# Optimization experiments

Measured on AMD Instinct MI355X. Metric: run time of the kernel, lower is better.

The kernel has to match this reference:

```python
import jax, jax.numpy as jnp
import numpy as np

D = 1024
H = 16
HD = D // H


def setup_inputs() -> dict:
    key = jax.random.key(0)
    ks = jax.random.split(key, 9)
    s = 1.0 / np.sqrt(D)
    x = jax.random.normal(ks[0], (2, 2048, D), dtype=jnp.float32)
    Wq = jax.random.uniform(ks[1], (D, D), jnp.float32, -s, s)
    bq = jax.random.uniform(ks[2], (D,), jnp.float32, -s, s)
    Wk = jax.random.uniform(ks[3], (D, D), jnp.float32, -s, s)
    bk = jax.random.uniform(ks[4], (D,), jnp.float32, -s, s)
    Wv = jax.random.uniform(ks[5], (D, D), jnp.float32, -s, s)
    bv = jax.random.uniform(ks[6], (D,), jnp.float32, -s, s)
    Wo = jax.random.uniform(ks[7], (D, D), jnp.float32, -s, s)
    bo = jax.random.uniform(ks[8], (D,), jnp.float32, -s, s)
    return {"x": x, "Wq": Wq, "bq": bq, "Wk": Wk, "bk": bk,
            "Wv": Wv, "bv": bv, "Wo": Wo, "bo": bo}


def reference(x, Wq, bq, Wk, bk, Wv, bv, Wo, bo):
    B, S, _ = x.shape
    # project and split heads -> [B, H, S, HD]
    def split(t):
        return t.reshape(B, S, H, HD).transpose(0, 2, 1, 3)
    q = split(x @ Wq + bq)
    k = split(x @ Wk + bk)
    v = split(x @ Wv + bv)
    scores = jnp.einsum('bhqd,bhkd->bhqk', q, k) / np.sqrt(HD).astype(np.float32)
    attn = jax.nn.softmax(scores, axis=-1)
    ctx = jnp.einsum('bhqk,bhkd->bhqd', attn, v)  # [B,H,S,HD]
    ctx = ctx.transpose(0, 2, 1, 3).reshape(B, S, D)
    return ctx @ Wo + bo
```

## Files before the change

### kernel.cpp

```cpp
#include <hip/hip_runtime.h>
#include <hip/hip_bf16.h>
#include <math.h>

#define BB 2
#define SS 2048
#define DD 1024
#define HH 16
#define HD 64
#define MM (BB * SS)

typedef __bf16 bf16;
typedef __attribute__((ext_vector_type(8))) __bf16 bf16x8;
typedef __attribute__((ext_vector_type(4))) __bf16 bf16x4;
typedef __attribute__((ext_vector_type(4))) float f32x4;

__device__ __forceinline__ void glds16(const bf16* g, bf16* l) {
    __builtin_amdgcn_global_load_lds(
        (const __attribute__((address_space(1))) void*)g,
        (__attribute__((address_space(3))) void*)l, 16, 0, 0);
}

__global__ __launch_bounds__(256) void cvt_x(const float* __restrict__ x,
                                             bf16* __restrict__ xb) {
    int i = (blockIdx.x * 256 + threadIdx.x) * 4;
    float4 v = *(const float4*)(x + i);
    bf16x4 o;
    o[0] = (bf16)v.x; o[1] = (bf16)v.y; o[2] = (bf16)v.z; o[3] = (bf16)v.w;
    *(bf16x4*)(xb + i) = o;
}

__global__ __launch_bounds__(256) void cvt_w(
    const float* __restrict__ W0, const float* __restrict__ W1,
    const float* __restrict__ W2, const float* __restrict__ W3,
    bf16* __restrict__ Wt) {
    const float* W = (blockIdx.z == 0) ? W0 : (blockIdx.z == 1) ? W1
                   : (blockIdx.z == 2) ? W2 : W3;
    bf16* dst = Wt + (size_t)blockIdx.z * DD * DD;

    __shared__ float T[64][65];
    int k0 = blockIdx.y * 64, n0 = blockIdx.x * 64;
    int tr = threadIdx.x >> 4, tc = (threadIdx.x & 15) * 4;
#pragma unroll
    for (int u = 0; u < 4; u++) {
        int r = tr + u * 16;
        float4 v = *(const float4*)&W[(size_t)(k0 + r) * DD + n0 + tc];
        T[tc + 0][r] = v.x; T[tc + 1][r] = v.y;
        T[tc + 2][r] = v.z; T[tc + 3][r] = v.w;
    }
    __syncthreads();
#pragma unroll
    for (int u = 0; u < 4; u++) {
        int r = tr + u * 16;
        bf16x4 o;
        o[0] = (bf16)T[r][tc + 0]; o[1] = (bf16)T[r][tc + 1];
        o[2] = (bf16)T[r][tc + 2]; o[3] = (bf16)T[r][tc + 3];
        *(bf16x4*)&dst[(size_t)(n0 + r) * DD + k0 + tc] = o;
    }
}

__global__ __launch_bounds__(256) void vt_kernel(const bf16* __restrict__ V,
                                                 bf16* __restrict__ Vt) {
    const int bh = blockIdx.y;
    const int b = bh >> 4, h = bh & 15;
    const int s0 = blockIdx.x * 64;

    __shared__ bf16 T[64][72];
    const int r = threadIdx.x >> 2;
    const int c0 = (threadIdx.x & 3) * 16;

    const bf16* src = V + ((size_t)(b * SS + s0 + r)) * DD + h * HD + c0;
    *(bf16x8*)&T[r][c0]     = *(const bf16x8*)(src);
    *(bf16x8*)&T[r][c0 + 8] = *(const bf16x8*)(src + 8);
    __syncthreads();

    bf16x8 o0, o1;
#pragma unroll
    for (int i = 0; i < 8; i++) o0[i] = T[c0 + i][r];
#pragma unroll
    for (int i = 0; i < 8; i++) o1[i] = T[c0 + 8 + i][r];
    bf16* dst = Vt + ((size_t)bh * HD + r) * SS + s0 + c0;
    *(bf16x8*)dst       = o0;
    *(bf16x8*)(dst + 8) = o1;
}

__global__ __launch_bounds__(256) void mfma_gemm(
    const bf16* __restrict__ A, const bf16* __restrict__ Wt0,
    const float* __restrict__ b0, const float* __restrict__ b1,
    const float* __restrict__ b2,
    bf16* __restrict__ o0, bf16* __restrict__ o1, bf16* __restrict__ o2,
    float* __restrict__ ofp32) {
    const int z = blockIdx.z;
    const bf16* Wt = Wt0 + (size_t)z * DD * DD;
    const float* bias = (z == 0) ? b0 : (z == 1) ? b1 : b2;
    bf16* dstb = (z == 0) ? o0 : (z == 1) ? o1 : o2;

    __shared__ __align__(16) bf16 As[128 * 64];
    __shared__ __align__(16) bf16 Bs[128 * 64];

    const int tid = threadIdx.x;
    const int lane = tid & 63;
    const int w = tid >> 6;
    const int l15 = lane & 15, quad = lane >> 4;
    const int m0 = blockIdx.y * 128;
    const int n0 = blockIdx.x * 128;
    const int mw = (w & 1) * 64;
    const int nw = (w >> 1) * 64;

    f32x4 acc[4][4];
#pragma unroll
    for (int i = 0; i < 4; i++)
#pragma unroll
        for (int j = 0; j < 4; j++) acc[i][j] = (f32x4){0.f, 0.f, 0.f, 0.f};

    for (int kt = 0; kt < DD; kt += 64) {
        __syncthreads();
#pragma unroll
        for (int u = 0; u < 4; u++) {
            int j = tid + u * 256;
            int row = j >> 3, cp = j & 7;
            int c = cp ^ (row & 7);
            glds16(A  + (size_t)(m0 + row) * DD + kt + c * 8, &As[j * 8]);
            glds16(Wt + (size_t)(n0 + row) * DD + kt + c * 8, &Bs[j * 8]);
        }
        __syncthreads();

#pragma unroll
        for (int kh = 0; kh < 2; kh++) {
            bf16x8 af[4], bf[4];
#pragma unroll
            for (int i = 0; i < 4; i++) {
                int ra = mw + i * 16 + l15;
                int ja = ra * 8 + ((kh * 4 + quad) ^ (ra & 7));
                af[i] = *(const bf16x8*)&As[ja * 8];
                int rb = nw + i * 16 + l15;
                int jb = rb * 8 + ((kh * 4 + quad) ^ (rb & 7));
                bf[i] = *(const bf16x8*)&Bs[jb * 8];
            }
#pragma unroll
            for (int i = 0; i < 4; i++)
#pragma unroll
                for (int j = 0; j < 4; j++)
                    acc[i][j] = __builtin_amdgcn_mfma_f32_16x16x32_bf16(
                        af[i], bf[j], acc[i][j], 0, 0, 0);
        }
    }

    float bcol[4];
#pragma unroll
    for (int j = 0; j < 4; j++) bcol[j] = bias[n0 + nw + j * 16 + l15];

    if (ofp32) {
#pragma unroll
        for (int i = 0; i < 4; i++)
#pragma unroll
            for (int j = 0; j < 4; j++)
#pragma unroll
                for (int r = 0; r < 4; r++) {
                    int row = m0 + mw + i * 16 + quad * 4 + r;
                    int col = n0 + nw + j * 16 + l15;
                    ofp32[(size_t)row * DD + col] = acc[i][j][r] + bcol[j];
                }
    } else {
#pragma unroll
        for (int i = 0; i < 4; i++)
#pragma unroll
            for (int j = 0; j < 4; j++)
#pragma unroll
                for (int r = 0; r < 4; r++) {
                    int row = m0 + mw + i * 16 + quad * 4 + r;
                    int col = n0 + nw + j * 16 + l15;
                    dstb[(size_t)row * DD + col] = (bf16)(acc[i][j][r] + bcol[j]);
                }
    }
}

__global__ __launch_bounds__(256) void mfma_attn(
    const bf16* __restrict__ Qb, const bf16* __restrict__ Kb,
    const bf16* __restrict__ Vtg, bf16* __restrict__ ctxb) {
    __shared__ __align__(16) bf16 Qs[64 * 64];
    __shared__ __align__(16) bf16 Ks[64 * 64];
    __shared__ __align__(16) bf16 Vs[64 * 64];
    __shared__ __align__(16) bf16 Ps[4][16 * 64];

    const int tid = threadIdx.x;
    const int lane = tid & 63;
    const int w = tid >> 6;
    const int l15 = lane & 15, quad = lane >> 4;
    const int bh = blockIdx.y;
    const int b = bh >> 4, h = bh & 15;
    const int q0 = blockIdx.x * 64;
    const size_t mb = (size_t)b * SS;
    const int hc = h * HD;
    const bf16* Vt_bh = Vtg + (size_t)bh * HD * SS;
    bf16* Pw = &Ps[w][0];

#pragma unroll
    for (int u = 0; u < 2; u++) {
        int j = tid + u * 256;
        int row = j >> 3, cp = j & 7;
        int c = cp ^ (row & 7);
        glds16(Qb + (mb + q0 + row) * DD + hc + c * 8, &Qs[j * 8]);
    }
    __syncthreads();

    bf16x8 qf[2];
    {
        int rq = w * 16 + l15;
#pragma unroll
        for (int kh = 0; kh < 2; kh++) {
            int jq = rq * 8 + ((kh * 4 + quad) ^ (rq & 7));
            qf[kh] = *(const bf16x8*)&Qs[jq * 8];
        }
    }

    float l_cur = 0.0f;
    f32x4 o[4];
#pragma unroll
    for (int nb = 0; nb < 4; nb++) o[nb] = (f32x4){0.f, 0.f, 0.f, 0.f};

    const float SCL = 0.18033688011112042f;

    int pw_off[4];
#pragma unroll
    for (int kb = 0; kb < 4; kb++) {
        int cw = kb * 2 + (quad >> 1);
        pw_off[kb] = l15 * 64 + ((cw ^ (l15 & 7)) << 3) + (quad & 1) * 4;
    }

    for (int kt = 0; kt < SS; kt += 64) {
        __syncthreads();
#pragma unroll
        for (int u = 0; u < 2; u++) {
            int j = tid + u * 256;
            int row = j >> 3, cp = j & 7;
            int c = cp ^ (row & 7);
            glds16(Kb + (mb + kt + row) * DD + hc + c * 8, &Ks[j * 8]);
            glds16(Vt_bh + (size_t)row * SS + kt + c * 8, &Vs[j * 8]);
        }
        __syncthreads();

        f32x4 sc[4];
#pragma unroll
        for (int kb = 0; kb < 4; kb++) sc[kb] = (f32x4){0.f, 0.f, 0.f, 0.f};
#pragma unroll
        for (int kb = 0; kb < 4; kb++) {
            int rk = kb * 16 + l15;
#pragma unroll
            for (int kh = 0; kh < 2; kh++) {
                int jk = rk * 8 + ((kh * 4 + quad) ^ (rk & 7));
                bf16x8 kf = *(const bf16x8*)&Ks[jk * 8];
                sc[kb] = __builtin_amdgcn_mfma_f32_16x16x32_bf16(
                    kf, qf[kh], sc[kb], 0, 0, 0);
            }
        }

        float rsum = 0.f;
#pragma unroll
        for (int kb = 0; kb < 4; kb++) {
            bf16x4 pvec;
#pragma unroll
            for (int r = 0; r < 4; r++) {
                float p = exp2f(sc[kb][r] * SCL);
                rsum += p;
                pvec[r] = (bf16)p;
            }
            *(bf16x4*)&Pw[pw_off[kb]] = pvec;
        }
        rsum += __shfl_xor(rsum, 16, 64);
        rsum += __shfl_xor(rsum, 32, 64);
        l_cur += rsum;

#pragma unroll
        for (int kh = 0; kh < 2; kh++) {
            bf16x8 pf = *(const bf16x8*)&Pw[l15 * 64 + (((kh * 4 + quad) ^ (l15 & 7)) << 3)];
#pragma unroll
            for (int nb = 0; nb < 4; nb++) {
                int rv = nb * 16 + l15;
                int jv = rv * 8 + ((kh * 4 + quad) ^ (rv & 7));
                bf16x8 vf = *(const bf16x8*)&Vs[jv * 8];
                o[nb] = __builtin_amdgcn_mfma_f32_16x16x32_bf16(
                    pf, vf, o[nb], 0, 0, 0);
            }
        }
    }

    float linv = 1.0f / l_cur;
    float li[4];
#pragma unroll
    for (int r = 0; r < 4; r++) li[r] = __shfl(linv, quad * 4 + r, 64);
#pragma unroll
    for (int nb = 0; nb < 4; nb++)
#pragma unroll
        for (int r = 0; r < 4; r++) {
            int qrow = q0 + w * 16 + quad * 4 + r;
            ctxb[(mb + qrow) * DD + hc + nb * 16 + l15] = (bf16)(o[nb][r] * li[r]);
        }
}

extern "C" void kernel_launch(void* const* d_in, const int* in_sizes, int n_in,
                              void* d_out, int out_size, void* d_ws, size_t ws_size,
                              hipStream_t stream) {
    const float* x  = (const float*)d_in[0];
    const float* Wq = (const float*)d_in[1];
    const float* bq = (const float*)d_in[2];
    const float* Wk = (const float*)d_in[3];
    const float* bk = (const float*)d_in[4];
    const float* Wv = (const float*)d_in[5];
    const float* bv = (const float*)d_in[6];
    const float* Wo = (const float*)d_in[7];
    const float* bo = (const float*)d_in[8];
    float* out = (float*)d_out;

    char* base = (char*)d_ws;
    bf16* xb   = (bf16*)(base);
    bf16* Wt   = (bf16*)(base + (8ull  << 20));
    bf16* Qb   = (bf16*)(base + (16ull << 20));
    bf16* Kb   = (bf16*)(base + (24ull << 20));
    bf16* Vb   = (bf16*)(base + (32ull << 20));
    bf16* ctxb = (bf16*)(base + (40ull << 20));
    bf16* Vtg  = xb;

    cvt_x<<<dim3((MM * DD) / (256 * 4)), dim3(256), 0, stream>>>(x, xb);
    cvt_w<<<dim3(16, 16, 4), dim3(256), 0, stream>>>(Wq, Wk, Wv, Wo, Wt);

    mfma_gemm<<<dim3(DD / 128, MM / 128, 3), dim3(256), 0, stream>>>(
        xb, Wt, bq, bk, bv, Qb, Kb, Vb, nullptr);

    vt_kernel<<<dim3(SS / 64, BB * HH), dim3(256), 0, stream>>>(Vb, Vtg);

    mfma_attn<<<dim3(SS / 64, BB * HH), dim3(256), 0, stream>>>(Qb, Kb, Vtg, ctxb);

    mfma_gemm<<<dim3(DD / 128, MM / 128, 1), dim3(256), 0, stream>>>(
        ctxb, Wt + 3ull * DD * DD, bo, bo, bo, nullptr, nullptr, nullptr, out);
}
```

Measured before the change: 229.8 us.

## Fold softmax scale into Q projection, add 64-row output GEMM, simplify attention addressing

The Q projection epilogue now multiplies by the softmax scale, so the attention inner loop drops one multiply per score. The output projection moves to a dedicated kernel with 64x128 tiles, doubling its grid from 256 to 512 blocks to fill more CUs. In the attention kernel, Q is loaded straight from global memory into registers instead of through shared memory, and the swizzled LDS offsets and global pointers are precomputed outside the KV loop. Scaling Q before the bf16 rounding slightly changes numerics, and the precomputed offsets raise register pressure.

Result: faster. 224.8 us (-2.2%).

```diff
diff --git a/kernel.cpp b/kernel.cpp
--- a/kernel.cpp
+++ b/kernel.cpp
@@ -13,6 +13,8 @@
 typedef __attribute__((ext_vector_type(8))) __bf16 bf16x8;
 typedef __attribute__((ext_vector_type(4))) __bf16 bf16x4;
 typedef __attribute__((ext_vector_type(4))) float f32x4;
+
+#define QSCL 0.18033688011112042f
 
 __device__ __forceinline__ void glds16(const bf16* g, bf16* l) {
     __builtin_amdgcn_global_load_lds(
@@ -87,12 +89,12 @@
     const bf16* __restrict__ A, const bf16* __restrict__ Wt0,
     const float* __restrict__ b0, const float* __restrict__ b1,
     const float* __restrict__ b2,
-    bf16* __restrict__ o0, bf16* __restrict__ o1, bf16* __restrict__ o2,
-    float* __restrict__ ofp32) {
+    bf16* __restrict__ o0, bf16* __restrict__ o1, bf16* __restrict__ o2) {
     const int z = blockIdx.z;
     const bf16* Wt = Wt0 + (size_t)z * DD * DD;
     const float* bias = (z == 0) ? b0 : (z == 1) ? b1 : b2;
     bf16* dstb = (z == 0) ? o0 : (z == 1) ? o1 : o2;
+    const float scl = (z == 0) ? QSCL : 1.0f;
 
     __shared__ __align__(16) bf16 As[128 * 64];
     __shared__ __align__(16) bf16 Bs[128 * 64];
@@ -149,35 +151,99 @@
 #pragma unroll
     for (int j = 0; j < 4; j++) bcol[j] = bias[n0 + nw + j * 16 + l15];
 
-    if (ofp32) {
-#pragma unroll
-        for (int i = 0; i < 4; i++)
-#pragma unroll
-            for (int j = 0; j < 4; j++)
-#pragma unroll
-                for (int r = 0; r < 4; r++) {
-                    int row = m0 + mw + i * 16 + quad * 4 + r;
-                    int col = n0 + nw + j * 16 + l15;
-                    ofp32[(size_t)row * DD + col] = acc[i][j][r] + bcol[j];
-                }
-    } else {
-#pragma unroll
-        for (int i = 0; i < 4; i++)
-#pragma unroll
-            for (int j = 0; j < 4; j++)
-#pragma unroll
-                for (int r = 0; r < 4; r++) {
-                    int row = m0 + mw + i * 16 + quad * 4 + r;
-                    int col = n0 + nw + j * 16 + l15;
-                    dstb[(size_t)row * DD + col] = (bf16)(acc[i][j][r] + bcol[j]);
-                }
-    }
+#pragma unroll
+    for (int i = 0; i < 4; i++)
+#pragma unroll
+        for (int j = 0; j < 4; j++)
+#pragma unroll
+            for (int r = 0; r < 4; r++) {
+                int row = m0 + mw + i * 16 + quad * 4 + r;
+                int col = n0 + nw + j * 16 + l15;
+                dstb[(size_t)row * DD + col] =
+                    (bf16)((acc[i][j][r] + bcol[j]) * scl);
+            }
+}
+
+__global__ __launch_bounds__(256) void mfma_gemm_out(
+    const bf16* __restrict__ A, const bf16* __restrict__ Wt,
+    const float* __restrict__ bias, float* __restrict__ out) {
+    __shared__ __align__(16) bf16 As[64 * 64];
+    __shared__ __align__(16) bf16 Bs[128 * 64];
+
+    const int tid = threadIdx.x;
+    const int lane = tid & 63;
+    const int w = tid >> 6;
+    const int l15 = lane & 15, quad = lane >> 4;
+    const int m0 = blockIdx.y * 64;
+    const int n0 = blockIdx.x * 128;
+    const int mw = (w & 1) * 32;
+    const int nw = (w >> 1) * 64;
+
+    f32x4 acc[2][4];
+#pragma unroll
+    for (int i = 0; i < 2; i++)
+#pragma unroll
+        for (int j = 0; j < 4; j++) acc[i][j] = (f32x4){0.f, 0.f, 0.f, 0.f};
+
+    for (int kt = 0; kt < DD; kt += 64) {
+        __syncthreads();
+#pragma unroll
+        for (int u = 0; u < 2; u++) {
+            int j = tid + u * 256;
+            int row = j >> 3, c = (j & 7) ^ (row & 7);
+            glds16(A + (size_t)(m0 + row) * DD + kt + c * 8, &As[j * 8]);
+        }
+#pragma unroll
+        for (int u = 0; u < 4; u++) {
+            int j = tid + u * 256;
+            int row = j >> 3, c = (j & 7) ^ (row & 7);
+            glds16(Wt + (size_t)(n0 + row) * DD + kt + c * 8, &Bs[j * 8]);
+        }
+        __syncthreads();
+
+#pragma unroll
+        for (int kh = 0; kh < 2; kh++) {
+            bf16x8 af[2], bf[4];
+#pragma unroll
+            for (int i = 0; i < 2; i++) {
+                int ra = mw + i * 16 + l15;
+                int ja = ra * 8 + ((kh * 4 + quad) ^ (ra & 7));
+                af[i] = *(const bf16x8*)&As[ja * 8];
+            }
+#pragma unroll
+            for (int j = 0; j < 4; j++) {
+                int rb = nw + j * 16 + l15;
+                int jb = rb * 8 + ((kh * 4 + quad) ^ (rb & 7));
+                bf[j] = *(const bf16x8*)&Bs[jb * 8];
+            }
+#pragma unroll
+            for (int i = 0; i < 2; i++)
+#pragma unroll
+                for (int j = 0; j < 4; j++)
+                    acc[i][j] = __builtin_amdgcn_mfma_f32_16x16x32_bf16(
+                        af[i], bf[j], acc[i][j], 0, 0, 0);
+        }
+    }
+
+    float bcol[4];
+#pragma unroll
+    for (int j = 0; j < 4; j++) bcol[j] = bias[n0 + nw + j * 16 + l15];
+
+#pragma unroll
+    for (int i = 0; i < 2; i++)
+#pragma unroll
+        for (int j = 0; j < 4; j++)
+#pragma unroll
+            for (int r = 0; r < 4; r++) {
+                int row = m0 + mw + i * 16 + quad * 4 + r;
+                int col = n0 + nw + j * 16 + l15;
+                out[(size_t)row * DD + col] = acc[i][j][r] + bcol[j];
+            }
 }
 
 __global__ __launch_bounds__(256) void mfma_attn(
     const bf16* __restrict__ Qb, const bf16* __restrict__ Kb,
     const bf16* __restrict__ Vtg, bf16* __restrict__ ctxb) {
-    __shared__ __align__(16) bf16 Qs[64 * 64];
     __shared__ __align__(16) bf16 Ks[64 * 64];
     __shared__ __align__(16) bf16 Vs[64 * 64];
     __shared__ __align__(16) bf16 Ps[4][16 * 64];
@@ -194,23 +260,47 @@
     const bf16* Vt_bh = Vtg + (size_t)bh * HD * SS;
     bf16* Pw = &Ps[w][0];
 
+    bf16x8 qf[2];
+#pragma unroll
+    for (int kh = 0; kh < 2; kh++)
+        qf[kh] = *(const bf16x8*)&Qb[(mb + q0 + w * 16 + l15) * DD +
+                                     hc + kh * 32 + quad * 8];
+
+    int koff[4][2], voff[4][2], prd[2], pwr[4];
+#pragma unroll
+    for (int kb = 0; kb < 4; kb++) {
+        int rk = kb * 16 + l15;
+#pragma unroll
+        for (int kh = 0; kh < 2; kh++)
+            koff[kb][kh] = (rk * 8 + ((kh * 4 + quad) ^ (rk & 7))) * 8;
+    }
+#pragma unroll
+    for (int nb = 0; nb < 4; nb++) {
+        int rv = nb * 16 + l15;
+#pragma unroll
+        for (int kh = 0; kh < 2; kh++)
+            voff[nb][kh] = (rv * 8 + ((kh * 4 + quad) ^ (rv & 7))) * 8;
+    }
+#pragma unroll
+    for (int kh = 0; kh < 2; kh++)
+        prd[kh] = l15 * 64 + (((kh * 4 + quad) ^ (l15 & 7)) << 3);
+#pragma unroll
+    for (int kb = 0; kb < 4; kb++) {
+        int cw = kb * 2 + (quad >> 1);
+        pwr[kb] = l15 * 64 + ((cw ^ (l15 & 7)) << 3) + (quad & 1) * 4;
+    }
+
+    const bf16* gK[2]; const bf16* gV[2];
+    bf16 *lK[2], *lV[2];
 #pragma unroll
     for (int u = 0; u < 2; u++) {
         int j = tid + u * 256;
         int row = j >> 3, cp = j & 7;
         int c = cp ^ (row & 7);
-        glds16(Qb + (mb + q0 + row) * DD + hc + c * 8, &Qs[j * 8]);
-    }
-    __syncthreads();
-
-    bf16x8 qf[2];
-    {
-        int rq = w * 16 + l15;
-#pragma unroll
-        for (int kh = 0; kh < 2; kh++) {
-            int jq = rq * 8 + ((kh * 4 + quad) ^ (rq & 7));
-            qf[kh] = *(const bf16x8*)&Qs[jq * 8];
-        }
+        gK[u] = Kb + (mb + row) * DD + hc + c * 8;
+        gV[u] = Vt_bh + (size_t)row * SS + c * 8;
+        lK[u] = &Ks[j * 8];
+        lV[u] = &Vs[j * 8];
     }
 
     float l_cur = 0.0f;
@@ -218,24 +308,12 @@
 #pragma unroll
     for (int nb = 0; nb < 4; nb++) o[nb] = (f32x4){0.f, 0.f, 0.f, 0.f};
 
-    const float SCL = 0.18033688011112042f;
-
-    int pw_off[4];
-#pragma unroll
-    for (int kb = 0; kb < 4; kb++) {
-        int cw = kb * 2 + (quad >> 1);
-        pw_off[kb] = l15 * 64 + ((cw ^ (l15 & 7)) << 3) + (quad & 1) * 4;
-    }
-
     for (int kt = 0; kt < SS; kt += 64) {
         __syncthreads();
 #pragma unroll
         for (int u = 0; u < 2; u++) {
-            int j = tid + u * 256;
-            int row = j >> 3, cp = j & 7;
-            int c = cp ^ (row & 7);
-            glds16(Kb + (mb + kt + row) * DD + hc + c * 8, &Ks[j * 8]);
-            glds16(Vt_bh + (size_t)row * SS + kt + c * 8, &Vs[j * 8]);
+            glds16(gK[u], lK[u]);  gK[u] += 64 * DD;
+            glds16(gV[u], lV[u]);  gV[u] += 64;
         }
         __syncthreads();
 
@@ -243,16 +321,13 @@
 #pragma unroll
         for (int kb = 0; kb < 4; kb++) sc[kb] = (f32x4){0.f, 0.f, 0.f, 0.f};
 #pragma unroll
-        for (int kb = 0; kb < 4; kb++) {
-            int rk = kb * 16 + l15;
+        for (int kb = 0; kb < 4; kb++)
 #pragma unroll
             for (int kh = 0; kh < 2; kh++) {
-                int jk = rk * 8 + ((kh * 4 + quad) ^ (rk & 7));
-                bf16x8 kf = *(const bf16x8*)&Ks[jk * 8];
+                bf16x8 kf = *(const bf16x8*)&Ks[koff[kb][kh]];
                 sc[kb] = __builtin_amdgcn_mfma_f32_16x16x32_bf16(
                     kf, qf[kh], sc[kb], 0, 0, 0);
             }
-        }
 
         float rsum = 0.f;
 #pragma unroll
@@ -260,11 +335,11 @@
             bf16x4 pvec;
 #pragma unroll
             for (int r = 0; r < 4; r++) {
-                float p = exp2f(sc[kb][r] * SCL);
+                float p = exp2f(sc[kb][r]);
                 rsum += p;
                 pvec[r] = (bf16)p;
             }
-            *(bf16x4*)&Pw[pw_off[kb]] = pvec;
+            *(bf16x4*)&Pw[pwr[kb]] = pvec;
         }
         rsum += __shfl_xor(rsum, 16, 64);
         rsum += __shfl_xor(rsum, 32, 64);
@@ -272,12 +347,10 @@
 
 #pragma unroll
         for (int kh = 0; kh < 2; kh++) {
-            bf16x8 pf = *(const bf16x8*)&Pw[l15 * 64 + (((kh * 4 + quad) ^ (l15 & 7)) << 3)];
+            bf16x8 pf = *(const bf16x8*)&Pw[prd[kh]];
 #pragma unroll
             for (int nb = 0; nb < 4; nb++) {
-                int rv = nb * 16 + l15;
-                int jv = rv * 8 + ((kh * 4 + quad) ^ (rv & 7));
-                bf16x8 vf = *(const bf16x8*)&Vs[jv * 8];
+                bf16x8 vf = *(const bf16x8*)&Vs[voff[nb][kh]];
                 o[nb] = __builtin_amdgcn_mfma_f32_16x16x32_bf16(
                     pf, vf, o[nb], 0, 0, 0);
             }
@@ -324,12 +397,12 @@
     cvt_w<<<dim3(16, 16, 4), dim3(256), 0, stream>>>(Wq, Wk, Wv, Wo, Wt);
 
     mfma_gemm<<<dim3(DD / 128, MM / 128, 3), dim3(256), 0, stream>>>(
-        xb, Wt, bq, bk, bv, Qb, Kb, Vb, nullptr);
+        xb, Wt, bq, bk, bv, Qb, Kb, Vb);
 
     vt_kernel<<<dim3(SS / 64, BB * HH), dim3(256), 0, stream>>>(Vb, Vtg);
 
     mfma_attn<<<dim3(SS / 64, BB * HH), dim3(256), 0, stream>>>(Qb, Kb, Vtg, ctxb);
 
-    mfma_gemm<<<dim3(DD / 128, MM / 128, 1), dim3(256), 0, stream>>>(
-        ctxb, Wt + 3ull * DD * DD, bo, bo, bo, nullptr, nullptr, nullptr, out);
-}
+    mfma_gemm_out<<<dim3(DD / 128, MM / 64), dim3(256), 0, stream>>>(
+        ctxb, Wt + 3ull * DD * DD, bo, out);
+}
```
